# Kernel optimization log

Hardware: AMD Instinct MI355X
Metric: run time of the kernel (lower is better)

The kernel has to match this reference:

```python
import jax, jax.numpy as jnp
import numpy as np

N, IN, OUT, T = 65536, 256, 256, 8


def setup_inputs() -> dict:
    key = jax.random.key(0)
    k1, k2, k3, k4 = jax.random.split(key, 4)
    x = jax.random.normal(k1, (N, IN), dtype=jnp.float32)
    types = jax.random.randint(k2, (N,), 0, T, dtype=jnp.int32)
    # xavier_uniform for W: limit = sqrt(6 / (fan_in + fan_out)) with fan computed
    # on the last two dims (out_size, in_size)
    limit = float(np.sqrt(6.0 / (IN + OUT)))
    W = jax.random.uniform(k3, (T, OUT, IN), dtype=jnp.float32, minval=-limit, maxval=limit)
    # original inits b to zeros; use small random values so the bias path is exercised
    b = 0.01 * jax.random.normal(k4, (T, OUT), dtype=jnp.float32)
    return {"x": x, "types": types, "W": W, "b": b}


def reference(x, types, W, b):
    # out[i] = W[types[i]] @ x[i] + b[types[i]]
    # Grouped-GEMM expressed as a loop over the small fixed set of types,
    # avoiding the huge [N, OUT, IN] gather of W[types].
    num_types = W.shape[0]
    out = b[types]  # [N, OUT]
    for t in range(num_types):
        mask = (types == t)[:, None]  # [N, 1]
        out = out + jnp.where(mask, x @ W[t].T, jnp.float32(0.0))
    return out
```

## Files before the change

### kernel.cpp

```cpp
#include <hip/hip_runtime.h>
#include <hip/hip_bf16.h>
#include <stdint.h>


#define NROWS 65536
#define NTYPES 8
#define KDIM 256
#define ODIM 256
#define BM 128
#define BN 128
#define BK 64
#define HB 64
#define MAXTILES 544

typedef __attribute__((ext_vector_type(8))) short short8;
typedef __attribute__((ext_vector_type(4))) float f32x4;

__device__ __forceinline__ unsigned short f2bf(float f) {
    unsigned int u = __float_as_uint(f);
    u += 0x7fffu + ((u >> 16) & 1u);
    return (unsigned short)(u >> 16);
}

__global__ void prep_hist_kernel(const int* __restrict__ types,
                                 const float* __restrict__ W,
                                 unsigned short* __restrict__ Wb,
                                 int* __restrict__ blockHist) {
    __shared__ int h[NTYPES];
    const int tid = threadIdx.x;
    if (tid < NTYPES) h[tid] = 0;
    __syncthreads();
    const int i = blockIdx.x * 1024 + tid;
    atomicAdd(&h[types[i]], 1);
    #pragma unroll
    for (int r = 0; r < 2; ++r) {
        int j = i + r * 65536;
        float4 v = ((const float4*)W)[j];
        ushort4 p;
        p.x = f2bf(v.x); p.y = f2bf(v.y); p.z = f2bf(v.z); p.w = f2bf(v.w);
        ((ushort4*)Wb)[j] = p;
    }
    __syncthreads();
    if (tid < NTYPES) blockHist[blockIdx.x * NTYPES + tid] = h[tid];
}

__global__ void scan_kernel(const int* __restrict__ blockHist,
                            int* __restrict__ blockBase,
                            int* __restrict__ typeBase,
                            int4* __restrict__ tiles,
                            int* __restrict__ tileCount) {
    __shared__ int scnt[NTYPES], sTypeBase[NTYPES], sTileBase[NTYPES + 1];
    const int tid = threadIdx.x;
    if (tid < NTYPES) {
        int run = 0;
        for (int b = 0; b < HB; ++b) {
            blockBase[b * NTYPES + tid] = run;
            run += blockHist[b * NTYPES + tid];
        }
        scnt[tid] = run;
    }
    __syncthreads();
    if (tid == 0) {
        int rowacc = 0, tileacc = 0;
        for (int t = 0; t < NTYPES; ++t) {
            sTypeBase[t] = rowacc; typeBase[t] = rowacc; rowacc += scnt[t];
            sTileBase[t] = tileacc; tileacc += (scnt[t] + BM - 1) / BM;
        }
        sTileBase[NTYPES] = tileacc;
        tileCount[0] = tileacc;
    }
    __syncthreads();
    const int tc = sTileBase[NTYPES];
    for (int j = tid; j < MAXTILES; j += 64) {
        if (j < tc) {
            int t = 0;
            while (t < NTYPES - 1 && j >= sTileBase[t + 1]) ++t;
            tiles[j] = make_int4(t, (j - sTileBase[t]) * BM, sTypeBase[t], scnt[t]);
        }
    }
}

__global__ void scatter_kernel(const int* __restrict__ types,
                               const int* __restrict__ blockBase,
                               const int* __restrict__ typeBase,
                               int* __restrict__ idx) {
    __shared__ int h[NTYPES];
    __shared__ int base[NTYPES];
    const int tid = threadIdx.x;
    if (tid < NTYPES) {
        h[tid] = 0;
        base[tid] = typeBase[tid] + blockBase[blockIdx.x * NTYPES + tid];
    }
    __syncthreads();
    const int i = blockIdx.x * 1024 + tid;
    const int t = types[i];
    int r = atomicAdd(&h[t], 1);
    idx[base[t] + r] = i;
}

__global__ __launch_bounds__(256, 2)
void gemm_kernel(const float* __restrict__ x,
                 const float* __restrict__ bias,
                 const unsigned short* __restrict__ Wb,
                 const int* __restrict__ tileCount,
                 const int4* __restrict__ tiles,
                 const int* __restrict__ idx,
                 float* __restrict__ out) {
    if ((int)blockIdx.x >= tileCount[0]) return;
    const int4 td = tiles[blockIdx.x];
    const int t = td.x, m0 = td.y, rbase = td.z, count = td.w;
    const int n0 = blockIdx.y * BN;
    const int rem = count - m0;

    __shared__ unsigned short As[2][BM * BK];
    __shared__ unsigned short Bs[2][BN * BK];

    const int tid = threadIdx.x;
    const int wave = tid >> 6;
    const int lane = tid & 63;
    const int lr = lane & 15;
    const int lq = lane >> 4;
    const int wm = (wave >> 1) * 64;
    const int wn = (wave & 1) * 64;

    const int* rowIdx = idx + rbase + m0;

    const int srow = tid >> 4;
    const int sc = tid & 15;
    const float* aptr[8];
    #pragma unroll
    for (int j = 0; j < 8; ++j) {
        int m = j * 16 + srow;
        aptr[j] = x + (size_t)rowIdx[m < rem ? m : 0] * KDIM + sc * 4;
    }

    float breg[4];
    #pragma unroll
    for (int j = 0; j < 4; ++j) breg[j] = bias[t * ODIM + n0 + wn + j * 16 + lr];

    const int bschunk = (lane & 7) ^ (lane >> 3);
    const unsigned short* bsrc0 = Wb + (size_t)t * ODIM * KDIM + (size_t)bschunk * 8;

    f32x4 acc[4][4] = {};
    float4 av[8];

#define ISSUE_B(buf, k0)                                                        \
    {                                                                           \
        _Pragma("unroll")                                                       \
        for (int it = 0; it < 4; ++it) {                                        \
            int dbyte = wave * 4096 + it * 1024;                                \
            int row = (dbyte >> 7) + (lane >> 3);                               \
            const unsigned short* src = bsrc0 + (size_t)(n0 + row) * KDIM + (k0); \
            __builtin_amdgcn_global_load_lds(                                   \
                (const __attribute__((address_space(1))) void*)src,             \
                (__attribute__((address_space(3))) void*)((char*)Bs[buf] + dbyte), \
                16, 0, 0);                                                      \
        }                                                                       \
    }

#define LOAD_A(k0)                                                              \
    {                                                                           \
        _Pragma("unroll")                                                       \
        for (int j = 0; j < 8; ++j) av[j] = *(const float4*)(aptr[j] + (k0));   \
    }

#define WRITE_A(buf)                                                            \
    {                                                                           \
        _Pragma("unroll")                                                       \
        for (int j = 0; j < 8; ++j) {                                           \
            int row = j * 16 + srow;                                            \
            ushort4 p;                                                          \
            p.x = f2bf(av[j].x); p.y = f2bf(av[j].y);                           \
            p.z = f2bf(av[j].z); p.w = f2bf(av[j].w);                           \
            int ch = (sc >> 1) ^ (row & 7);                                     \
            *(ushort4*)((char*)As[buf] + row * 128 + ch * 16 + (sc & 1) * 8) = p; \
        }                                                                       \
    }

    ISSUE_B(0, 0);
    LOAD_A(0);
    WRITE_A(0);
    __syncthreads();

    #pragma unroll
    for (int i = 0; i < 4; ++i) {
        const int cur = i & 1;
        if (i < 3) {
            ISSUE_B(cur ^ 1, (i + 1) * BK);
            LOAD_A((i + 1) * BK);
        }
        #pragma unroll
        for (int kh = 0; kh < 2; ++kh) {
            short8 af[4], bfr[4];
            #pragma unroll
            for (int q = 0; q < 4; ++q) {
                int arow = wm + q * 16 + lr;
                int ach = ((kh << 2) + lq) ^ (arow & 7);
                af[q] = *(const short8*)((char*)As[cur] + arow * 128 + ach * 16);
            }
            #pragma unroll
            for (int q = 0; q < 4; ++q) {
                int brow = wn + q * 16 + lr;
                int bch = ((kh << 2) + lq) ^ (brow & 7);
                bfr[q] = *(const short8*)((char*)Bs[cur] + brow * 128 + bch * 16);
            }
            #pragma unroll
            for (int q = 0; q < 4; ++q)
                #pragma unroll
                for (int j = 0; j < 4; ++j)
                    acc[q][j] = __builtin_amdgcn_mfma_f32_16x16x32_bf16(
                        af[q], bfr[j], acc[q][j], 0, 0, 0);
        }
        if (i < 3) {
            WRITE_A(cur ^ 1);
            __syncthreads();
        }
    }

    #pragma unroll
    for (int q = 0; q < 4; ++q) {
        #pragma unroll
        for (int r = 0; r < 4; ++r) {
            int lm = wm + q * 16 + lq * 4 + r;
            if (lm < rem) {
                size_t orow = (size_t)rowIdx[lm] * ODIM + n0;
                #pragma unroll
                for (int j = 0; j < 4; ++j)
                    out[orow + wn + j * 16 + lr] = acc[q][j][r] + breg[j];
            }
        }
    }
#undef ISSUE_B
#undef LOAD_A
#undef WRITE_A
}

extern "C" void kernel_launch(void* const* d_in, const int* in_sizes, int n_in,
                              void* d_out, int out_size, void* d_ws, size_t ws_size,
                              hipStream_t stream) {
    const float* x     = (const float*)d_in[0];
    const int*   types = (const int*)d_in[1];
    const float* W     = (const float*)d_in[2];
    const float* b     = (const float*)d_in[3];
    float* out = (float*)d_out;

    char* ws = (char*)d_ws;
    int*  tileCount = (int*)ws;
    int*  typeBase  = (int*)(ws + 128);
    int*  blockHist = (int*)(ws + 512);
    int*  blockBase = (int*)(ws + 2560);
    int4* tiles     = (int4*)(ws + 4608);
    int*  idx       = (int*)(ws + 16384);
    unsigned short* Wb = (unsigned short*)(ws + 278528);

    prep_hist_kernel<<<HB, 1024, 0, stream>>>(types, W, Wb, blockHist);
    scan_kernel<<<1, 64, 0, stream>>>(blockHist, blockBase, typeBase, tiles, tileCount);
    scatter_kernel<<<HB, 1024, 0, stream>>>(types, blockBase, typeBase, idx);
    gemm_kernel<<<dim3(MAXTILES, 2), 256, 0, stream>>>(x, b, Wb, tileCount, tiles, idx, out);
}
```

Before: 144.6 us.

## Widen GEMM tile to full output width, drop double buffering, parallelize scan

The GEMM now uses 512-thread blocks that each cover all 256 output columns, so every gathered x row is loaded and converted to bf16 once instead of twice. The double-buffered LDS pipeline is replaced by a single buffer with two barriers per K step, cutting LDS use so that more blocks can be resident. The histogram and scatter kernels move to 256-thread blocks with more blocks, and the scan becomes a shuffle-based parallel prefix sum over 256 threads. The risk is lost overlap of global loads with MFMA work, since there is no longer any prefetch.

```diff
diff --git a/kernel.cpp b/kernel.cpp
--- a/kernel.cpp
+++ b/kernel.cpp
@@ -8,10 +8,10 @@
 #define KDIM 256
 #define ODIM 256
 #define BM 128
-#define BN 128
+#define BN 256
 #define BK 64
-#define HB 64
-#define MAXTILES 544
+#define HB 256
+#define MAXTILES 640
 
 typedef __attribute__((ext_vector_type(8))) short short8;
 typedef __attribute__((ext_vector_type(4))) float f32x4;
@@ -22,19 +22,19 @@
     return (unsigned short)(u >> 16);
 }
 
-__global__ void prep_hist_kernel(const int* __restrict__ types,
-                                 const float* __restrict__ W,
-                                 unsigned short* __restrict__ Wb,
-                                 int* __restrict__ blockHist) {
+__global__ void hist_kernel(const int* __restrict__ types,
+                            const float* __restrict__ W,
+                            unsigned short* __restrict__ Wb,
+                            int* __restrict__ blockHist) {
     __shared__ int h[NTYPES];
     const int tid = threadIdx.x;
     if (tid < NTYPES) h[tid] = 0;
     __syncthreads();
-    const int i = blockIdx.x * 1024 + tid;
+    const int i = blockIdx.x * 256 + tid;
     atomicAdd(&h[types[i]], 1);
     #pragma unroll
     for (int r = 0; r < 2; ++r) {
-        int j = i + r * 65536;
+        int j = blockIdx.x * 512 + r * 256 + tid;
         float4 v = ((const float4*)W)[j];
         ushort4 p;
         p.x = f2bf(v.x); p.y = f2bf(v.y); p.z = f2bf(v.z); p.w = f2bf(v.w);
@@ -49,34 +49,50 @@
                             int* __restrict__ typeBase,
                             int4* __restrict__ tiles,
                             int* __restrict__ tileCount) {
-    __shared__ int scnt[NTYPES], sTypeBase[NTYPES], sTileBase[NTYPES + 1];
-    const int tid = threadIdx.x;
-    if (tid < NTYPES) {
-        int run = 0;
-        for (int b = 0; b < HB; ++b) {
-            blockBase[b * NTYPES + tid] = run;
-            run += blockHist[b * NTYPES + tid];
-        }
-        scnt[tid] = run;
-    }
-    __syncthreads();
+    __shared__ int v[HB * NTYPES];
+    __shared__ int scnt[NTYPES];
+    __shared__ int sTypeBase[NTYPES], sTileBase[NTYPES + 1];
+    const int tid = threadIdx.x;
+    for (int j = tid; j < HB * NTYPES; j += 256) v[j] = blockHist[j];
+    __syncthreads();
+
+    const int t = tid >> 5;
+    const int l = tid & 31;
+    int s[8];
+    int sum = 0;
+    #pragma unroll
+    for (int m = 0; m < 8; ++m) {
+        s[m] = sum;
+        sum += v[(l * 8 + m) * NTYPES + t];
+    }
+    int incl = sum;
+    #pragma unroll
+    for (int d = 1; d < 32; d <<= 1) {
+        int y = __shfl_up(incl, d, 32);
+        if (l >= d) incl += y;
+    }
+    const int excl = incl - sum;
+    #pragma unroll
+    for (int m = 0; m < 8; ++m)
+        blockBase[(l * 8 + m) * NTYPES + t] = excl + s[m];
+    if (l == 31) scnt[t] = incl;
+    __syncthreads();
+
     if (tid == 0) {
         int rowacc = 0, tileacc = 0;
-        for (int t = 0; t < NTYPES; ++t) {
-            sTypeBase[t] = rowacc; typeBase[t] = rowacc; rowacc += scnt[t];
-            sTileBase[t] = tileacc; tileacc += (scnt[t] + BM - 1) / BM;
+        for (int q = 0; q < NTYPES; ++q) {
+            sTypeBase[q] = rowacc; typeBase[q] = rowacc; rowacc += scnt[q];
+            sTileBase[q] = tileacc; tileacc += (scnt[q] + BM - 1) / BM;
         }
         sTileBase[NTYPES] = tileacc;
         tileCount[0] = tileacc;
     }
     __syncthreads();
     const int tc = sTileBase[NTYPES];
-    for (int j = tid; j < MAXTILES; j += 64) {
-        if (j < tc) {
-            int t = 0;
-            while (t < NTYPES - 1 && j >= sTileBase[t + 1]) ++t;
-            tiles[j] = make_int4(t, (j - sTileBase[t]) * BM, sTypeBase[t], scnt[t]);
-        }
+    for (int j = tid; j < tc; j += 256) {
+        int q = 0;
+        while (q < NTYPES - 1 && j >= sTileBase[q + 1]) ++q;
+        tiles[j] = make_int4(q, (j - sTileBase[q]) * BM, sTypeBase[q], scnt[q]);
     }
 }
 
@@ -92,13 +108,13 @@
         base[tid] = typeBase[tid] + blockBase[blockIdx.x * NTYPES + tid];
     }
     __syncthreads();
-    const int i = blockIdx.x * 1024 + tid;
+    const int i = blockIdx.x * 256 + tid;
     const int t = types[i];
     int r = atomicAdd(&h[t], 1);
     idx[base[t] + r] = i;
 }
 
-__global__ __launch_bounds__(256, 2)
+__global__ __launch_bounds__(512, 4)
 void gemm_kernel(const float* __restrict__ x,
                  const float* __restrict__ bias,
                  const unsigned short* __restrict__ Wb,
@@ -109,86 +125,63 @@
     if ((int)blockIdx.x >= tileCount[0]) return;
     const int4 td = tiles[blockIdx.x];
     const int t = td.x, m0 = td.y, rbase = td.z, count = td.w;
-    const int n0 = blockIdx.y * BN;
     const int rem = count - m0;
 
-    __shared__ unsigned short As[2][BM * BK];
-    __shared__ unsigned short Bs[2][BN * BK];
+    __shared__ unsigned short As[BM * BK];
+    __shared__ unsigned short Bs[BN * BK];
 
     const int tid = threadIdx.x;
     const int wave = tid >> 6;
     const int lane = tid & 63;
     const int lr = lane & 15;
     const int lq = lane >> 4;
-    const int wm = (wave >> 1) * 64;
-    const int wn = (wave & 1) * 64;
+    const int wm = (wave & 1) * 64;
+    const int wn = (wave >> 1) * 64;
 
     const int* rowIdx = idx + rbase + m0;
 
     const int srow = tid >> 4;
     const int sc = tid & 15;
-    const float* aptr[8];
-    #pragma unroll
-    for (int j = 0; j < 8; ++j) {
-        int m = j * 16 + srow;
+    const float* aptr[4];
+    #pragma unroll
+    for (int j = 0; j < 4; ++j) {
+        int m = j * 32 + srow;
         aptr[j] = x + (size_t)rowIdx[m < rem ? m : 0] * KDIM + sc * 4;
     }
 
     float breg[4];
     #pragma unroll
-    for (int j = 0; j < 4; ++j) breg[j] = bias[t * ODIM + n0 + wn + j * 16 + lr];
+    for (int j = 0; j < 4; ++j) breg[j] = bias[t * ODIM + wn + j * 16 + lr];
 
     const int bschunk = (lane & 7) ^ (lane >> 3);
     const unsigned short* bsrc0 = Wb + (size_t)t * ODIM * KDIM + (size_t)bschunk * 8;
 
     f32x4 acc[4][4] = {};
-    float4 av[8];
-
-#define ISSUE_B(buf, k0)                                                        \
-    {                                                                           \
-        _Pragma("unroll")                                                       \
-        for (int it = 0; it < 4; ++it) {                                        \
-            int dbyte = wave * 4096 + it * 1024;                                \
-            int row = (dbyte >> 7) + (lane >> 3);                               \
-            const unsigned short* src = bsrc0 + (size_t)(n0 + row) * KDIM + (k0); \
-            __builtin_amdgcn_global_load_lds(                                   \
-                (const __attribute__((address_space(1))) void*)src,             \
-                (__attribute__((address_space(3))) void*)((char*)Bs[buf] + dbyte), \
-                16, 0, 0);                                                      \
-        }                                                                       \
-    }
-
-#define LOAD_A(k0)                                                              \
-    {                                                                           \
-        _Pragma("unroll")                                                       \
-        for (int j = 0; j < 8; ++j) av[j] = *(const float4*)(aptr[j] + (k0));   \
-    }
-
-#define WRITE_A(buf)                                                            \
-    {                                                                           \
-        _Pragma("unroll")                                                       \
-        for (int j = 0; j < 8; ++j) {                                           \
-            int row = j * 16 + srow;                                            \
-            ushort4 p;                                                          \
-            p.x = f2bf(av[j].x); p.y = f2bf(av[j].y);                           \
-            p.z = f2bf(av[j].z); p.w = f2bf(av[j].w);                           \
-            int ch = (sc >> 1) ^ (row & 7);                                     \
-            *(ushort4*)((char*)As[buf] + row * 128 + ch * 16 + (sc & 1) * 8) = p; \
-        }                                                                       \
-    }
-
-    ISSUE_B(0, 0);
-    LOAD_A(0);
-    WRITE_A(0);
-    __syncthreads();
-
-    #pragma unroll
-    for (int i = 0; i < 4; ++i) {
-        const int cur = i & 1;
-        if (i < 3) {
-            ISSUE_B(cur ^ 1, (i + 1) * BK);
-            LOAD_A((i + 1) * BK);
-        }
+    char* AsB = (char*)As;
+    char* BsB = (char*)Bs;
+
+    for (int k0 = 0; k0 < KDIM; k0 += BK) {
+        #pragma unroll
+        for (int it = 0; it < 4; ++it) {
+            int dbyte = it * 8192 + wave * 1024;
+            int row = (dbyte >> 7) + (lane >> 3);
+            const unsigned short* src = bsrc0 + (size_t)row * KDIM + k0;
+            __builtin_amdgcn_global_load_lds(
+                (const __attribute__((address_space(1))) void*)src,
+                (__attribute__((address_space(3))) void*)(BsB + dbyte),
+                16, 0, 0);
+        }
+        #pragma unroll
+        for (int j = 0; j < 4; ++j) {
+            int row = j * 32 + srow;
+            const float4 v = *(const float4*)(aptr[j] + k0);
+            ushort4 p;
+            p.x = f2bf(v.x); p.y = f2bf(v.y); p.z = f2bf(v.z); p.w = f2bf(v.w);
+            int ch = (sc >> 1) ^ (row & 7);
+            *(ushort4*)(AsB + row * 128 + ch * 16 + (sc & 1) * 8) = p;
+        }
+        __syncthreads();
+
         #pragma unroll
         for (int kh = 0; kh < 2; ++kh) {
             short8 af[4], bfr[4];
@@ -196,13 +189,13 @@
             for (int q = 0; q < 4; ++q) {
                 int arow = wm + q * 16 + lr;
                 int ach = ((kh << 2) + lq) ^ (arow & 7);
-                af[q] = *(const short8*)((char*)As[cur] + arow * 128 + ach * 16);
+                af[q] = *(const short8*)(AsB + arow * 128 + ach * 16);
             }
             #pragma unroll
             for (int q = 0; q < 4; ++q) {
                 int brow = wn + q * 16 + lr;
                 int bch = ((kh << 2) + lq) ^ (brow & 7);
-                bfr[q] = *(const short8*)((char*)Bs[cur] + brow * 128 + bch * 16);
+                bfr[q] = *(const short8*)(BsB + brow * 128 + bch * 16);
             }
             #pragma unroll
             for (int q = 0; q < 4; ++q)
@@ -211,10 +204,7 @@
                     acc[q][j] = __builtin_amdgcn_mfma_f32_16x16x32_bf16(
                         af[q], bfr[j], acc[q][j], 0, 0, 0);
         }
-        if (i < 3) {
-            WRITE_A(cur ^ 1);
-            __syncthreads();
-        }
+        __syncthreads();
     }
 
     #pragma unroll
@@ -223,16 +213,13 @@
         for (int r = 0; r < 4; ++r) {
             int lm = wm + q * 16 + lq * 4 + r;
             if (lm < rem) {
-                size_t orow = (size_t)rowIdx[lm] * ODIM + n0;
+                size_t orow = (size_t)rowIdx[lm] * ODIM;
                 #pragma unroll
                 for (int j = 0; j < 4; ++j)
                     out[orow + wn + j * 16 + lr] = acc[q][j][r] + breg[j];
             }
         }
     }
-#undef ISSUE_B
-#undef LOAD_A
-#undef WRITE_A
 }
 
 extern "C" void kernel_launch(void* const* d_in, const int* in_sizes, int n_in,
@@ -248,13 +235,13 @@
     int*  tileCount = (int*)ws;
     int*  typeBase  = (int*)(ws + 128);
     int*  blockHist = (int*)(ws + 512);
-    int*  blockBase = (int*)(ws + 2560);
-    int4* tiles     = (int4*)(ws + 4608);
-    int*  idx       = (int*)(ws + 16384);
-    unsigned short* Wb = (unsigned short*)(ws + 278528);
-
-    prep_hist_kernel<<<HB, 1024, 0, stream>>>(types, W, Wb, blockHist);
-    scan_kernel<<<1, 64, 0, stream>>>(blockHist, blockBase, typeBase, tiles, tileCount);
-    scatter_kernel<<<HB, 1024, 0, stream>>>(types, blockBase, typeBase, idx);
-    gemm_kernel<<<dim3(MAXTILES, 2), 256, 0, stream>>>(x, b, Wb, tileCount, tiles, idx, out);
-}
+    int*  blockBase = (int*)(ws + 9216);
+    int4* tiles     = (int4*)(ws + 17408);
+    int*  idx       = (int*)(ws + 32768);
+    unsigned short* Wb = (unsigned short*)(ws + 294912);
+
+    hist_kernel<<<HB, 256, 0, stream>>>(types, W, Wb, blockHist);
+    scan_kernel<<<1, 256, 0, stream>>>(blockHist, blockBase, typeBase, tiles, tileCount);
+    scatter_kernel<<<HB, 256, 0, stream>>>(types, blockBase, typeBase, idx);
+    gemm_kernel<<<dim3(MAXTILES, 1), 512, 0, stream>>>(x, b, Wb, tileCount, tiles, idx, out);
+}
```

Result: no change. 143.9 us (-0.5%).
